# Kernel tuning notes

Measured on AMD Instinct MI355X. Metric: run time of the kernel, lower is better.

The kernel has to match this reference:

```python
import jax, jax.numpy as jnp
import numpy as np

HEADS = 16
EPS = 1e-6


def _rmsnorm(x, gamma):
    # x: [..., head_dim]
    inv = jax.lax.rsqrt(jnp.mean(x * x, axis=-1, keepdims=True) + EPS)
    return x * inv * gamma


def setup_inputs() -> dict:
    key = jax.random.key(0)
    ks = jax.random.split(key, 7)
    B, L, Lc, D, CTX = 4, 4096, 1024, 1024, 1024
    hd = D // HEADS
    s = 1.0 / np.sqrt(D)
    return {
        "x": jax.random.normal(ks[0], (B, L, D), jnp.float32),
        "ctx": jax.random.normal(ks[1], (B, Lc, CTX), jnp.float32),
        "Wq": jax.random.normal(ks[2], (D, D), jnp.float32) * s,
        "Wkv": jax.random.normal(ks[3], (CTX, 2 * D), jnp.float32) * s,
        "Wproj": jax.random.normal(ks[4], (D, D), jnp.float32) * s,
        "q_gamma": jnp.ones((hd,), jnp.float32),
        "k_gamma": jnp.ones((hd,), jnp.float32),
    }


def reference(x, ctx, Wq, Wkv, Wproj, q_gamma, k_gamma):
    B, L, D = x.shape
    Lc = ctx.shape[1]
    H = HEADS
    hd = D // H
    # projections
    q = (x @ Wq).reshape(B, L, H, hd).transpose(0, 2, 1, 3)        # [B,H,L,hd]
    kv = (ctx @ Wkv).reshape(B, Lc, 2, H, hd).transpose(2, 0, 3, 1, 4)
    k, v = kv[0], kv[1]                                            # [B,H,Lc,hd]
    # per-head QK RMSNorm
    q = _rmsnorm(q, q_gamma)
    k = _rmsnorm(k, k_gamma)
    scale = 1.0 / np.sqrt(hd)
    attn = jnp.einsum("bhld,bhmd->bhlm", q, k) * scale             # [B,H,L,Lc]
    attn = jax.nn.softmax(attn, axis=-1)
    out = jnp.einsum("bhlm,bhmd->bhld", attn, v)                   # [B,H,L,hd]
    out = out.transpose(0, 2, 1, 3).reshape(B, L, D)
    return out @ Wproj
```

## Files before the change

kernel.cpp:

```cpp
#include <hip/hip_runtime.h>

typedef __bf16 bf16x8 __attribute__((ext_vector_type(8)));
typedef __bf16 bf16x4 __attribute__((ext_vector_type(4)));
typedef float f32x4 __attribute__((ext_vector_type(4)));

__device__ __forceinline__ void gl_lds16(const void* g, void* l) {
  __builtin_amdgcn_global_load_lds(
      (const __attribute__((address_space(1))) unsigned int*)g,
      (__attribute__((address_space(3))) unsigned int*)l, 16, 0, 0);
}

__global__ __launch_bounds__(256) void conv_bf16_kernel(
    const float* __restrict__ in, __bf16* __restrict__ out, int n4) {
  int i = blockIdx.x * 256 + threadIdx.x;
  if (i < n4) {
    float4 v = ((const float4*)in)[i];
    bf16x4 o;
    o[0] = (__bf16)v.x; o[1] = (__bf16)v.y; o[2] = (__bf16)v.z; o[3] = (__bf16)v.w;
    *(bf16x4*)(out + (size_t)i * 4) = o;
  }
}

__global__ __launch_bounds__(256) void tconv_kernel(
    const float* __restrict__ W, __bf16* __restrict__ Wt, int R, int C) {
  __shared__ float t[32][33];
  int c0 = blockIdx.x * 32, r0 = blockIdx.y * 32;
  int tx = threadIdx.x, ty = threadIdx.y;
#pragma unroll
  for (int i = 0; i < 4; ++i)
    t[ty + i * 8][tx] = W[(size_t)(r0 + ty + i * 8) * C + c0 + tx];
  __syncthreads();
#pragma unroll
  for (int i = 0; i < 4; ++i)
    Wt[(size_t)(c0 + ty + i * 8) * R + r0 + tx] = (__bf16)t[tx][ty + i * 8];
}

template <int NORM, int OUTF32>
__global__ __launch_bounds__(256) void gemm_kernel(
    const __bf16* __restrict__ A, const __bf16* __restrict__ Bt,
    void* __restrict__ Cout, void* __restrict__ Cout2,
    int M, int N, int K, const float* __restrict__ gamma) {
  __shared__ alignas(16) __bf16 Alds[2][128 * 32];
  __shared__ alignas(16) __bf16 Blds[2][128 * 32];
  const int tid = threadIdx.x;
  const int w = tid >> 6, l = tid & 63;
  const int lg = l & 15, lh = l >> 4;
  const int wr = w >> 1, wc = w & 1;
  const int brow = blockIdx.y * 128, bcol = blockIdx.x * 128;

  const f32x4 zero = {0.f, 0.f, 0.f, 0.f};
  f32x4 acc[4][4];
#pragma unroll
  for (int m = 0; m < 4; ++m)
#pragma unroll
    for (int n = 0; n < 4; ++n) acc[m][n] = zero;

  auto STAGE = [&](int buf, int k0) {
#pragma unroll
    for (int j = 0; j < 2; ++j) {
      int c = j * 256 + w * 64 + l;
      gl_lds16(A + (size_t)(brow + (c >> 2)) * K + k0 + (c & 3) * 8,
               (char*)Alds[buf] + (j * 256 + w * 64) * 16);
      gl_lds16(Bt + (size_t)(bcol + (c >> 2)) * K + k0 + (c & 3) * 8,
               (char*)Blds[buf] + (j * 256 + w * 64) * 16);
    }
  };

  STAGE(0, 0);
  __syncthreads();
  for (int k0 = 0; k0 < K; k0 += 32) {
    int cur = (k0 >> 5) & 1;
    if (k0 + 32 < K) STAGE(cur ^ 1, k0 + 32);
    bf16x8 af[4], bfr[4];
#pragma unroll
    for (int m = 0; m < 4; ++m)
      af[m] = *(const bf16x8*)(Alds[cur] + (wr * 64 + m * 16 + lg) * 32 + lh * 8);
#pragma unroll
    for (int n = 0; n < 4; ++n)
      bfr[n] = *(const bf16x8*)(Blds[cur] + (wc * 64 + n * 16 + lg) * 32 + lh * 8);
#pragma unroll
    for (int m = 0; m < 4; ++m)
#pragma unroll
      for (int n = 0; n < 4; ++n)
        acc[m][n] = __builtin_amdgcn_mfma_f32_16x16x32_bf16(af[m], bfr[n], acc[m][n], 0, 0, 0);
    __syncthreads();
  }

  const int col64 = bcol + wc * 64;
  if (NORM == 1 || (NORM == 2 && col64 < 1024)) {
    float gm[4];
#pragma unroll
    for (int n = 0; n < 4; ++n) gm[n] = gamma[n * 16 + lg];
#pragma unroll
    for (int m = 0; m < 4; ++m) {
#pragma unroll
      for (int i = 0; i < 4; ++i) {
        float ss = 0.f;
#pragma unroll
        for (int n = 0; n < 4; ++n) ss += acc[m][n][i] * acc[m][n][i];
        ss += __shfl_xor(ss, 1);
        ss += __shfl_xor(ss, 2);
        ss += __shfl_xor(ss, 4);
        ss += __shfl_xor(ss, 8);
        float inv = rsqrtf(ss * (1.0f / 64.0f) + 1e-6f);
#pragma unroll
        for (int n = 0; n < 4; ++n) acc[m][n][i] *= inv * gm[n];
      }
    }
  }

  if (NORM == 2) {
    if (col64 < 1024) {
#pragma unroll
      for (int m = 0; m < 4; ++m)
#pragma unroll
        for (int n = 0; n < 4; ++n)
#pragma unroll
          for (int i = 0; i < 4; ++i) {
            size_t idx = (size_t)(brow + wr * 64 + m * 16 + lh * 4 + i) * 1024 +
                         col64 + n * 16 + lg;
            ((__bf16*)Cout)[idx] = (__bf16)acc[m][n][i];
          }
    } else {
#pragma unroll
      for (int m = 0; m < 4; ++m) {
        int row = brow + wr * 64 + m * 16 + lh * 4;
        int bb = row >> 10, kv0 = row & 1023;
        int g = kv0 & 31;
        int pos = (kv0 & ~31) + ((g & 15) >> 2) * 8 + (g >> 4) * 4;
#pragma unroll
        for (int n = 0; n < 4; ++n) {
          int col = col64 + n * 16 + lg - 1024;
          bf16x4 v;
#pragma unroll
          for (int i = 0; i < 4; ++i) v[i] = (__bf16)acc[m][n][i];
          *(bf16x4*)((__bf16*)Cout2 + ((size_t)(bb * 1024 + col)) * 1024 + pos) = v;
        }
      }
    }
    return;
  }

#pragma unroll
  for (int m = 0; m < 4; ++m)
#pragma unroll
    for (int n = 0; n < 4; ++n)
#pragma unroll
      for (int i = 0; i < 4; ++i) {
        size_t idx = (size_t)(brow + wr * 64 + m * 16 + lh * 4 + i) * N +
                     bcol + wc * 64 + n * 16 + lg;
        if (OUTF32) ((float*)Cout)[idx] = acc[m][n][i];
        else ((__bf16*)Cout)[idx] = (__bf16)acc[m][n][i];
      }
}

__global__ __launch_bounds__(512) void flash_kernel(
    const __bf16* __restrict__ Qb, const __bf16* __restrict__ Kb,
    const __bf16* __restrict__ Vt, __bf16* __restrict__ Ob) {
  const int orig = blockIdx.x;
  const int wgid = (orig & 7) * 128 + (orig >> 3);
  const int qt = wgid & 15, h = (wgid >> 4) & 15, b = wgid >> 8;
  const int tid = threadIdx.x;
  const int w = tid >> 6, l = tid & 63, lg = l & 15, lh = l >> 4;
  __shared__ alignas(16) char lds[32768];

  const int qrow0 = b * 4096 + qt * 256 + w * 32;
  bf16x8 qfr[2][2];
#pragma unroll
  for (int mff = 0; mff < 2; ++mff)
#pragma unroll
    for (int dc = 0; dc < 2; ++dc)
      qfr[mff][dc] = *(const bf16x8*)(Qb + (size_t)(qrow0 + mff * 16 + lg) * 1024 +
                                      h * 64 + dc * 32 + lh * 8);

  const char* Kg = (const char*)Kb + (size_t)b * 2097152 + h * 128;
  const char* Vg = (const char*)Vt + (size_t)(b * 16 + h) * 64 * 2048;

  const int o16 = tid * 16;
  const int op = o16 ^ (((o16 >> 7) & 7) << 4);
  const int srow = op >> 7, scb = op & 127;

  auto STAGE = [&](int buf, int kt) {
    gl_lds16(Kg + (size_t)(kt * 64 + srow) * 2048 + scb, lds + buf * 8192 + w * 1024);
    gl_lds16(Vg + (size_t)srow * 2048 + kt * 128 + scb, lds + 16384 + buf * 8192 + w * 1024);
  };

  const int swz = (lg & 7) << 4;
  const int off0 = lg * 128 + ((lh * 16) ^ swz);
  const int off1 = lg * 128 + (((64 + lh * 16)) ^ swz);

  const f32x4 zero = {0.f, 0.f, 0.f, 0.f};
  f32x4 o_[4][2];
  float m_[2], lp_[2];
#pragma unroll
  for (int df = 0; df < 4; ++df)
#pragma unroll
    for (int qf = 0; qf < 2; ++qf) o_[df][qf] = zero;
  m_[0] = m_[1] = -1e30f;
  lp_[0] = lp_[1] = 0.f;

  const float C = 0.18033688f;
  const float DT = 44.361f;

  STAGE(0, 0);
  __syncthreads();
#pragma unroll 2
  for (int kt = 0; kt < 16; ++kt) {
    const int cur = kt & 1;
    const char* Kc = lds + cur * 8192;
    const char* Vc = lds + 16384 + cur * 8192;
    if (kt < 15) STAGE(cur ^ 1, kt + 1);

    f32x4 st[4][2];
#pragma unroll
    for (int kvf = 0; kvf < 4; ++kvf)
#pragma unroll
      for (int mff = 0; mff < 2; ++mff) st[kvf][mff] = zero;
    __builtin_amdgcn_s_setprio(1);
#pragma unroll
    for (int dc = 0; dc < 2; ++dc)
#pragma unroll
      for (int kvf = 0; kvf < 4; ++kvf) {
        bf16x8 kf = *(const bf16x8*)(Kc + (dc ? off1 : off0) + kvf * 2048);
#pragma unroll
        for (int mff = 0; mff < 2; ++mff)
          st[kvf][mff] = __builtin_amdgcn_mfma_f32_16x16x32_bf16(kf, qfr[mff][dc], st[kvf][mff], 0, 0, 0);
      }
    __builtin_amdgcn_s_setprio(0);

    float pmax[2];
#pragma unroll
    for (int qf = 0; qf < 2; ++qf) {
      float ma[4];
#pragma unroll
      for (int i = 0; i < 4; ++i)
        ma[i] = fmaxf(fmaxf(st[0][qf][i], st[1][qf][i]),
                      fmaxf(st[2][qf][i], st[3][qf][i]));
      float t = fmaxf(fmaxf(ma[0], ma[1]), fmaxf(ma[2], ma[3]));
      t = fmaxf(t, __shfl_xor(t, 16));
      t = fmaxf(t, __shfl_xor(t, 32));
      pmax[qf] = t;
    }

    int need = (pmax[0] - m_[0] > DT) || (pmax[1] - m_[1] > DT);
    if (__any(need)) {
#pragma unroll
      for (int qf = 0; qf < 2; ++qf) {
        float nm = fmaxf(m_[qf], pmax[qf]);
        float r = __builtin_amdgcn_exp2f((m_[qf] - nm) * C);
        m_[qf] = nm;
        lp_[qf] *= r;
#pragma unroll
        for (int df = 0; df < 4; ++df)
#pragma unroll
          for (int i = 0; i < 4; ++i) o_[df][qf][i] *= r;
      }
    }

    bf16x4 pb[4][2];
#pragma unroll
    for (int qf = 0; qf < 2; ++qf) {
      float rs = 0.f;
      float mc = -m_[qf] * C;
#pragma unroll
      for (int kvf = 0; kvf < 4; ++kvf) {
#pragma unroll
        for (int i = 0; i < 4; ++i) {
          float p = __builtin_amdgcn_exp2f(fmaf(st[kvf][qf][i], C, mc));
          pb[kvf][qf][i] = (__bf16)p;
          rs += p;
        }
      }
      lp_[qf] += rs;
    }

    __builtin_amdgcn_s_setprio(1);
#pragma unroll
    for (int p = 0; p < 2; ++p) {
      union { bf16x4 h[2]; bf16x8 v; } pc[2];
#pragma unroll
      for (int qf = 0; qf < 2; ++qf) {
        pc[qf].h[0] = pb[2 * p][qf];
        pc[qf].h[1] = pb[2 * p + 1][qf];
      }
#pragma unroll
      for (int df = 0; df < 4; ++df) {
        bf16x8 vv = *(const bf16x8*)(Vc + (p ? off1 : off0) + df * 2048);
#pragma unroll
        for (int qf = 0; qf < 2; ++qf)
          o_[df][qf] = __builtin_amdgcn_mfma_f32_16x16x32_bf16(vv, pc[qf].v, o_[df][qf], 0, 0, 0);
      }
    }
    __builtin_amdgcn_s_setprio(0);

    asm volatile("s_waitcnt vmcnt(0)" ::: "memory");
    __syncthreads();
  }

#pragma unroll
  for (int qf = 0; qf < 2; ++qf) {
    float ls = lp_[qf];
    ls += __shfl_xor(ls, 16);
    ls += __shfl_xor(ls, 32);
    float inv = 1.f / ls;
    size_t qrow = (size_t)(qrow0 + qf * 16 + lg) * 1024 + h * 64;
#pragma unroll
    for (int df = 0; df < 4; ++df) {
      bf16x4 ov;
#pragma unroll
      for (int i = 0; i < 4; ++i) ov[i] = (__bf16)(o_[df][qf][i] * inv);
      *(bf16x4*)(Ob + qrow + df * 16 + lh * 4) = ov;
    }
  }
}

extern "C" void kernel_launch(void* const* d_in, const int* in_sizes, int n_in,
                              void* d_out, int out_size, void* d_ws, size_t ws_size,
                              hipStream_t stream) {
  const float* x     = (const float*)d_in[0];
  const float* ctx   = (const float*)d_in[1];
  const float* Wq    = (const float*)d_in[2];
  const float* Wkv   = (const float*)d_in[3];
  const float* Wproj = (const float*)d_in[4];
  const float* qg    = (const float*)d_in[5];
  const float* kg    = (const float*)d_in[6];
  float* out = (float*)d_out;

  char* ws = (char*)d_ws;
  __bf16* xb   = (__bf16*)(ws);
  __bf16* cb   = (__bf16*)(ws + (size_t)32 * 1048576);
  __bf16* Wqt  = (__bf16*)(ws + (size_t)40 * 1048576);
  __bf16* Wkvt = (__bf16*)(ws + (size_t)42 * 1048576);
  __bf16* Wpt  = (__bf16*)(ws + (size_t)46 * 1048576);
  __bf16* Qb   = (__bf16*)(ws + (size_t)48 * 1048576);
  __bf16* Kb   = (__bf16*)(ws + (size_t)80 * 1048576);
  __bf16* Vt   = (__bf16*)(ws + (size_t)88 * 1048576);
  __bf16* Ob   = xb;

  conv_bf16_kernel<<<16384, 256, 0, stream>>>(x, xb, 4194304);
  conv_bf16_kernel<<<4096, 256, 0, stream>>>(ctx, cb, 1048576);
  tconv_kernel<<<dim3(32, 32), dim3(32, 8), 0, stream>>>(Wq, Wqt, 1024, 1024);
  tconv_kernel<<<dim3(64, 32), dim3(32, 8), 0, stream>>>(Wkv, Wkvt, 1024, 2048);
  tconv_kernel<<<dim3(32, 32), dim3(32, 8), 0, stream>>>(Wproj, Wpt, 1024, 1024);

  gemm_kernel<1, 0><<<dim3(8, 128), 256, 0, stream>>>(xb, Wqt, Qb, nullptr, 16384, 1024, 1024, qg);
  gemm_kernel<2, 0><<<dim3(16, 32), 256, 0, stream>>>(cb, Wkvt, Kb, Vt, 4096, 2048, 1024, kg);
  flash_kernel<<<1024, 512, 0, stream>>>(Qb, Kb, Vt, Ob);
  gemm_kernel<0, 1><<<dim3(8, 128), 256, 0, stream>>>(Ob, Wpt, out, nullptr, 16384, 1024, 1024, nullptr);
}
```

Measured before the change: 277.8 us.

## Stage two KV tiles per barrier in flash kernel and swizzle GEMM block order

The flash attention kernel now processes KV tiles in pairs. It prefetches the next two tiles into a four-slot LDS buffer (64 KB) and issues only one wait-and-barrier per pair, so there are half as many synchronisations per block. Separately, the GEMM kernel remaps its block index so that groups of eight consecutive launched blocks are spread across the grid in strided chunks, which is meant to improve cache locality across compute units. The larger LDS footprint can lower occupancy of the flash kernel to one block per CU.

After: 258.0 us. 7.2% less time.

```diff
diff --git a/kernel.cpp b/kernel.cpp
--- a/kernel.cpp
+++ b/kernel.cpp
@@ -46,7 +46,12 @@
   const int w = tid >> 6, l = tid & 63;
   const int lg = l & 15, lh = l >> 4;
   const int wr = w >> 1, wc = w & 1;
-  const int brow = blockIdx.y * 128, bcol = blockIdx.x * 128;
+
+  const int nbx = gridDim.x;
+  const int lid = blockIdx.y * nbx + blockIdx.x;
+  const int cpx = (nbx * gridDim.y) >> 3;
+  const int swz = (lid & 7) * cpx + (lid >> 3);
+  const int brow = (swz / nbx) * 128, bcol = (swz % nbx) * 128;
 
   const f32x4 zero = {0.f, 0.f, 0.f, 0.f};
   f32x4 acc[4][4];
@@ -162,7 +167,7 @@
   const int qt = wgid & 15, h = (wgid >> 4) & 15, b = wgid >> 8;
   const int tid = threadIdx.x;
   const int w = tid >> 6, l = tid & 63, lg = l & 15, lh = l >> 4;
-  __shared__ alignas(16) char lds[32768];
+  __shared__ alignas(16) char lds[65536];
 
   const int qrow0 = b * 4096 + qt * 256 + w * 32;
   bf16x8 qfr[2][2];
@@ -182,12 +187,12 @@
 
   auto STAGE = [&](int buf, int kt) {
     gl_lds16(Kg + (size_t)(kt * 64 + srow) * 2048 + scb, lds + buf * 8192 + w * 1024);
-    gl_lds16(Vg + (size_t)srow * 2048 + kt * 128 + scb, lds + 16384 + buf * 8192 + w * 1024);
+    gl_lds16(Vg + (size_t)srow * 2048 + kt * 128 + scb, lds + 32768 + buf * 8192 + w * 1024);
   };
 
-  const int swz = (lg & 7) << 4;
-  const int off0 = lg * 128 + ((lh * 16) ^ swz);
-  const int off1 = lg * 128 + (((64 + lh * 16)) ^ swz);
+  const int swzl = (lg & 7) << 4;
+  const int off0 = lg * 128 + ((lh * 16) ^ swzl);
+  const int off1 = lg * 128 + ((64 + lh * 16) ^ swzl);
 
   const f32x4 zero = {0.f, 0.f, 0.f, 0.f};
   f32x4 o_[4][2];
@@ -202,15 +207,7 @@
   const float C = 0.18033688f;
   const float DT = 44.361f;
 
-  STAGE(0, 0);
-  __syncthreads();
-#pragma unroll 2
-  for (int kt = 0; kt < 16; ++kt) {
-    const int cur = kt & 1;
-    const char* Kc = lds + cur * 8192;
-    const char* Vc = lds + 16384 + cur * 8192;
-    if (kt < 15) STAGE(cur ^ 1, kt + 1);
-
+  auto COMPUTE = [&](const char* Kc, const char* Vc) {
     f32x4 st[4][2];
 #pragma unroll
     for (int kvf = 0; kvf < 4; ++kvf)
@@ -277,11 +274,11 @@
     __builtin_amdgcn_s_setprio(1);
 #pragma unroll
     for (int p = 0; p < 2; ++p) {
-      union { bf16x4 h[2]; bf16x8 v; } pc[2];
+      union { bf16x4 hv[2]; bf16x8 v; } pc[2];
 #pragma unroll
       for (int qf = 0; qf < 2; ++qf) {
-        pc[qf].h[0] = pb[2 * p][qf];
-        pc[qf].h[1] = pb[2 * p + 1][qf];
+        pc[qf].hv[0] = pb[2 * p][qf];
+        pc[qf].hv[1] = pb[2 * p + 1][qf];
       }
 #pragma unroll
       for (int df = 0; df < 4; ++df) {
@@ -292,7 +289,20 @@
       }
     }
     __builtin_amdgcn_s_setprio(0);
-
+  };
+
+  STAGE(0, 0);
+  STAGE(1, 1);
+  __syncthreads();
+#pragma unroll 2
+  for (int it = 0; it < 8; ++it) {
+    const int pb_ = (it & 1) * 2;
+    if (it < 7) {
+      STAGE(pb_ ^ 2, 2 * it + 2);
+      STAGE((pb_ ^ 2) + 1, 2 * it + 3);
+    }
+    COMPUTE(lds + pb_ * 8192, lds + 32768 + pb_ * 8192);
+    COMPUTE(lds + (pb_ + 1) * 8192, lds + 32768 + (pb_ + 1) * 8192);
     asm volatile("s_waitcnt vmcnt(0)" ::: "memory");
     __syncthreads();
   }
```
